# Performance work log

Measured on AMD Instinct MI355X. Metric: run time of the kernel, lower is better.

Reference implementation:

```python
import jax, jax.numpy as jnp
import numpy as np

T, B = 64, 512
X, H, Z, A = 1024, 1024, 256, 64


def setup_inputs() -> dict:
    key = jax.random.key(0)
    ks = jax.random.split(key, 24)
    s = 0.02
    n = lambda k, shape: (jax.random.normal(k, shape, dtype=jnp.float32) * s)
    d = {
        "obs_seq": jax.random.normal(ks[0], (T, B, X), dtype=jnp.float32),
        "act_seq": jax.random.normal(ks[1], (T, B, A), dtype=jnp.float32),
        "eps": jax.random.normal(ks[2], (T, B, Z), dtype=jnp.float32),
        # Transition: aggr Linear(z+a -> h), GRUCell(h, h)
        "aggr_W": n(ks[3], (Z + A, H)), "aggr_b": jnp.zeros((H,), jnp.float32),
        "gru_Wih": n(ks[4], (H, 3 * H)), "gru_Whh": n(ks[5], (H, 3 * H)),
        "gru_bih": jnp.zeros((3 * H,), jnp.float32), "gru_bhh": jnp.zeros((3 * H,), jnp.float32),
        # z_q_dist: NormalPredictor(x+h -> hidden h -> z)
        "q_W1": n(ks[6], (X + H, H)), "q_b1": jnp.zeros((H,), jnp.float32),
        "q_Wm": n(ks[7], (H, Z)), "q_bm": jnp.zeros((Z,), jnp.float32),
        "q_Ws": n(ks[8], (H, Z)), "q_bs": jnp.zeros((Z,), jnp.float32),
        # z_p_dist: NormalPredictor(h -> hidden h -> z)
        "p_W1": n(ks[9], (H, H)), "p_b1": jnp.zeros((H,), jnp.float32),
        "p_Wm": n(ks[10], (H, Z)), "p_bm": jnp.zeros((Z,), jnp.float32),
        "p_Ws": n(ks[11], (H, Z)), "p_bs": jnp.zeros((Z,), jnp.float32),
    }
    return d


def _gru_cell(x, h, Wih, Whh, bih, bhh):
    # torch.nn.GRUCell math
    gi = x @ Wih + bih
    gh = h @ Whh + bhh
    i_r, i_z, i_n = jnp.split(gi, 3, axis=-1)
    h_r, h_z, h_n = jnp.split(gh, 3, axis=-1)
    r = jax.nn.sigmoid(i_r + h_r)
    z = jax.nn.sigmoid(i_z + h_z)
    n = jnp.tanh(i_n + r * h_n)
    return (1.0 - z) * n + z * h


def _normal_predictor(x, W1, b1, Wm, bm, Ws, bs):
    hid = jax.nn.elu(x @ W1 + b1)
    loc = hid @ Wm + bm
    scale = jax.nn.softplus(hid @ Ws + bs)
    return loc, scale


def reference(obs_seq, act_seq, eps, aggr_W, aggr_b, gru_Wih, gru_Whh, gru_bih,
              gru_bhh, q_W1, q_b1, q_Wm, q_bm, q_Ws, q_bs, p_W1, p_b1, p_Wm,
              p_bm, p_Ws, p_bs):
    batch = obs_seq.shape[1]
    h0 = jnp.zeros((batch, gru_Whh.shape[0]), dtype=obs_seq.dtype)

    def step(h, inp):
        obs, act, e = inp
        q_loc, q_scale = _normal_predictor(
            jnp.concatenate([obs, h], axis=-1), q_W1, q_b1, q_Wm, q_bm, q_Ws, q_bs)
        z_q = q_loc + q_scale * e  # rsample
        p_loc, p_scale = _normal_predictor(h, p_W1, p_b1, p_Wm, p_bm, p_Ws, p_bs)
        a = jax.nn.elu(jnp.concatenate([z_q, act], axis=-1) @ aggr_W + aggr_b)
        h_new = _gru_cell(a, h, gru_Wih, gru_Whh, gru_bih, gru_bhh)
        return h_new, (h_new, q_loc, q_scale, p_loc, p_scale, z_q)

    _, (bel, q_loc, q_scale, p_loc, p_scale, z_qs) = jax.lax.scan(
        step, h0, (obs_seq, act_seq, eps))
    beliefs = jnp.concatenate([h0[None], bel], axis=0)  # [T+1, B, H]
    return beliefs, (q_loc, q_scale), (p_loc, p_scale), z_qs
```

## Files before the change

### kernel.cpp

```cpp
#include <hip/hip_runtime.h>
#include <hip/hip_bf16.h>
#include <stdint.h>

#define TT 64
#define BB 512
#define XX 1024
#define HH 1024
#define ZZ 256
#define AA 64

typedef __bf16 bf16;
typedef bf16 bf16x8 __attribute__((ext_vector_type(8)));
typedef float f32x4 __attribute__((ext_vector_type(4)));

#define SZ_BEL ((long)(TT + 1) * BB * HH)
#define SZ_TBZ ((long)TT * BB * ZZ)
#define OFF_QL (SZ_BEL)
#define OFF_QS (OFF_QL + SZ_TBZ)
#define OFF_PL (OFF_QL + 2 * SZ_TBZ)
#define OFF_PS (OFF_QL + 3 * SZ_TBZ)
#define OFF_ZQ (OFF_QL + 4 * SZ_TBZ)

#define GLL16(g, l)                                                         \
  __builtin_amdgcn_global_load_lds(                                         \
      (__attribute__((address_space(1))) void*)(g),                         \
      (__attribute__((address_space(3))) void*)(l), 16, 0, 0)

__device__ __forceinline__ float eluf(float x) {
  return x > 0.f ? x : expf(x) - 1.f;
}
__device__ __forceinline__ float splusf(float x) {
  return fmaxf(x, 0.f) + log1pf(expf(-fabsf(x)));
}
__device__ __forceinline__ float sigf(float x) {
  return 1.f / (1.f + expf(-x));
}

struct GArgs {
  const bf16* A; const float* Af; const bf16* A2;
  long lda, lda2; int ksplit;
  const bf16* Bt;
  int M, N, K, t;
  const float *b_q1, *b_ghh, *b_ag, *b_p1, *b_pm, *b_ps;
  const bf16* obs_pre;
  bf16 *hid_q, *a_buf, *out_bf;
  float *gh, *dout;
};

template <int BM, int BN, int EPI, bool AF32>
__global__ __launch_bounds__(256) void gemm_k(GArgs g) {
  constexpr int BK = 32;
  constexpr int WTM = BM / 2, WTN = BN / 2;
  constexpr int MR = WTM / 16, NR = WTN / 16;
  constexpr int CA = BM * 4 / 256, CB = BN * 4 / 256;
  __shared__ bf16 sA[BM * BK];
  __shared__ bf16 sB[BN * BK];
  const int nbm = g.M / BM;
  const int bm = blockIdx.x % nbm, bn = blockIdx.x / nbm;
  const int m0 = bm * BM, n0 = bn * BN;
  const int tid = threadIdx.x;
  const int wid = tid >> 6, lane = tid & 63;
  const int wm = wid & 1, wn = wid >> 1;
  const int lr = lane & 15, lk = lane >> 4;

  f32x4 acc[MR][NR] = {};

  for (int k0 = 0; k0 < g.K; k0 += BK) {
    __syncthreads();
    if constexpr (AF32) {
#pragma unroll
      for (int i = 0; i < CA; i++) {
        int c = tid + i * 256, row = c >> 2, kc = c & 3;
        const float* s = g.Af + (long)(m0 + row) * g.lda + k0 + kc * 8;
        float4 v0 = *(const float4*)s;
        float4 v1 = *(const float4*)(s + 4);
        bf16x8 p;
        p[0] = (bf16)v0.x; p[1] = (bf16)v0.y; p[2] = (bf16)v0.z; p[3] = (bf16)v0.w;
        p[4] = (bf16)v1.x; p[5] = (bf16)v1.y; p[6] = (bf16)v1.z; p[7] = (bf16)v1.w;
        *(bf16x8*)&sA[c * 8] = p;
      }
    } else {
#pragma unroll
      for (int i = 0; i < CA; i++) {
        int c = tid + i * 256, row = c >> 2, kc = c & 3;
        const bf16* s;
        if (EPI == 3 && k0 >= g.ksplit)
          s = g.A2 + (long)(m0 + row) * g.lda2 + (k0 - g.ksplit) + kc * 8;
        else
          s = g.A + (long)(m0 + row) * g.lda + k0 + kc * 8;
        GLL16(s, &sA[c * 8]);
      }
    }
#pragma unroll
    for (int i = 0; i < CB; i++) {
      int c = tid + i * 256, row = c >> 2, kc = c & 3;
      GLL16(g.Bt + (long)(n0 + row) * g.K + k0 + kc * 8, &sB[c * 8]);
    }
    __syncthreads();
    bf16x8 af[MR];
#pragma unroll
    for (int mi = 0; mi < MR; mi++)
      af[mi] = *(const bf16x8*)&sA[(wm * WTM + mi * 16 + lr) * BK + lk * 8];
#pragma unroll
    for (int nj = 0; nj < NR; nj++) {
      bf16x8 bfr = *(const bf16x8*)&sB[(wn * WTN + nj * 16 + lr) * BK + lk * 8];
#pragma unroll
      for (int mi = 0; mi < MR; mi++)
        acc[mi][nj] = __builtin_amdgcn_mfma_f32_16x16x32_bf16(af[mi], bfr, acc[mi][nj], 0, 0, 0);
    }
  }

#pragma unroll
  for (int mi = 0; mi < MR; mi++) {
#pragma unroll
    for (int nj = 0; nj < NR; nj++) {
#pragma unroll
      for (int r = 0; r < 4; r++) {
        const int row = m0 + wm * WTM + mi * 16 + lk * 4 + r;
        const int col = n0 + wn * WTN + nj * 16 + lr;
        float v = acc[mi][nj][r];
        if constexpr (EPI == 0) {
          g.out_bf[(long)row * g.N + col] = (bf16)v;
        } else if constexpr (EPI == 1) {
          if (col < HH) {
            float x = v + g.b_q1[col] + (float)g.obs_pre[((long)g.t * BB + row) * HH + col];
            g.hid_q[row * HH + col] = (bf16)eluf(x);
          } else {
            int j = col - HH;
            g.gh[(long)row * 3 * HH + j] = v + g.b_ghh[j];
          }
        } else if constexpr (EPI == 3) {
          g.a_buf[row * HH + col] = (bf16)eluf(v + g.b_ag[col]);
        } else if constexpr (EPI == 5) {
          g.out_bf[(long)row * g.N + col] = (bf16)eluf(v + g.b_p1[col]);
        } else {
          int region = col >> 8, j = col & 255;
          float x = v + (region ? g.b_ps[j] : g.b_pm[j]);
          if (region) x = splusf(x);
          g.dout[(region ? OFF_PS : OFF_PL) + (long)row * ZZ + j] = x;
        }
      }
    }
  }
}

struct QZArgs {
  const bf16* A; const bf16* Bt2;
  const float *b_qm, *b_qs; const float* eps;
  float* dout; bf16* z_bf; int t;
};
__global__ __launch_bounds__(256) void qz_gemm(QZArgs g) {
  constexpr int BK = 32;
  __shared__ bf16 sA[64 * BK];
  __shared__ bf16 sB[256 * BK];
  const int bm = blockIdx.x & 7, bn = blockIdx.x >> 3;
  const int m0 = bm * 64, n0 = bn * 128;
  const int tid = threadIdx.x;
  const int wid = tid >> 6, lane = tid & 63;
  const int wm = wid & 1, wn = wid >> 1;
  const int lr = lane & 15, lk = lane >> 4;

  f32x4 accL[2][4] = {}, accS[2][4] = {};

  for (int k0 = 0; k0 < HH; k0 += BK) {
    __syncthreads();
    {
      int c = tid, row = c >> 2, kc = c & 3;
      GLL16(g.A + (long)(m0 + row) * HH + k0 + kc * 8, &sA[c * 8]);
    }
#pragma unroll
    for (int i = 0; i < 4; i++) {
      int c = tid + i * 256, row = c >> 2, kc = c & 3;
      int grow = (row < 128) ? (n0 + row) : (256 + n0 + (row - 128));
      GLL16(g.Bt2 + (long)grow * HH + k0 + kc * 8, &sB[c * 8]);
    }
    __syncthreads();
    bf16x8 af[2];
#pragma unroll
    for (int mi = 0; mi < 2; mi++)
      af[mi] = *(const bf16x8*)&sA[(wm * 32 + mi * 16 + lr) * BK + lk * 8];
#pragma unroll
    for (int nj = 0; nj < 4; nj++) {
      bf16x8 bL = *(const bf16x8*)&sB[(wn * 64 + nj * 16 + lr) * BK + lk * 8];
      bf16x8 bS = *(const bf16x8*)&sB[(128 + wn * 64 + nj * 16 + lr) * BK + lk * 8];
#pragma unroll
      for (int mi = 0; mi < 2; mi++) {
        accL[mi][nj] = __builtin_amdgcn_mfma_f32_16x16x32_bf16(af[mi], bL, accL[mi][nj], 0, 0, 0);
        accS[mi][nj] = __builtin_amdgcn_mfma_f32_16x16x32_bf16(af[mi], bS, accS[mi][nj], 0, 0, 0);
      }
    }
  }

#pragma unroll
  for (int mi = 0; mi < 2; mi++) {
#pragma unroll
    for (int nj = 0; nj < 4; nj++) {
#pragma unroll
      for (int r = 0; r < 4; r++) {
        const int row = m0 + wm * 32 + mi * 16 + lk * 4 + r;
        const int j = n0 + wn * 64 + nj * 16 + lr;
        long o = ((long)g.t * BB + row) * ZZ + j;
        float loc = accL[mi][nj][r] + g.b_qm[j];
        float sc = splusf(accS[mi][nj][r] + g.b_qs[j]);
        float z = loc + sc * g.eps[o];
        g.dout[OFF_QL + o] = loc;
        g.dout[OFF_QS + o] = sc;
        g.dout[OFF_ZQ + o] = z;
        g.z_bf[row * ZZ + j] = (bf16)z;
      }
    }
  }
}

struct GRUArgs {
  const bf16* A; const bf16* Bt;
  const float* b_gih; const float* gh;
  bf16* h_bf; float* dout; int t;
};
__global__ __launch_bounds__(256) void gru_gemm(GRUArgs g) {
  constexpr int BK = 32;
  __shared__ bf16 sA[64 * BK];
  __shared__ bf16 sB[192 * BK];
  const int bm = blockIdx.x & 7, bn = blockIdx.x >> 3;
  const int m0 = bm * 64, n0 = bn * 64;
  const int tid = threadIdx.x;
  const int wid = tid >> 6, lane = tid & 63;
  const int wm = wid & 1, wn = wid >> 1;
  const int lr = lane & 15, lk = lane >> 4;

  f32x4 acc[2][3][2] = {};

  for (int k0 = 0; k0 < HH; k0 += BK) {
    __syncthreads();
    {
      int c = tid, row = c >> 2, kc = c & 3;
      GLL16(g.A + (long)(m0 + row) * HH + k0 + kc * 8, &sA[c * 8]);
    }
#pragma unroll
    for (int i = 0; i < 3; i++) {
      int c = tid + i * 256, row = c >> 2, kc = c & 3;
      int gate = row >> 6, jr = row & 63;
      GLL16(g.Bt + (long)(gate * HH + n0 + jr) * HH + k0 + kc * 8, &sB[c * 8]);
    }
    __syncthreads();
    bf16x8 af[2];
#pragma unroll
    for (int mi = 0; mi < 2; mi++)
      af[mi] = *(const bf16x8*)&sA[(wm * 32 + mi * 16 + lr) * BK + lk * 8];
#pragma unroll
    for (int gt = 0; gt < 3; gt++) {
#pragma unroll
      for (int nj = 0; nj < 2; nj++) {
        bf16x8 bfr = *(const bf16x8*)&sB[(gt * 64 + wn * 32 + nj * 16 + lr) * BK + lk * 8];
#pragma unroll
        for (int mi = 0; mi < 2; mi++)
          acc[mi][gt][nj] = __builtin_amdgcn_mfma_f32_16x16x32_bf16(af[mi], bfr, acc[mi][gt][nj], 0, 0, 0);
      }
    }
  }

#pragma unroll
  for (int mi = 0; mi < 2; mi++) {
#pragma unroll
    for (int nj = 0; nj < 2; nj++) {
#pragma unroll
      for (int r = 0; r < 4; r++) {
        const int row = m0 + wm * 32 + mi * 16 + lk * 4 + r;
        const int j = n0 + wn * 32 + nj * 16 + lr;
        const long gb = (long)row * 3 * HH + j;
        float gir = acc[mi][0][nj][r] + g.b_gih[j];
        float giz = acc[mi][1][nj][r] + g.b_gih[HH + j];
        float gin = acc[mi][2][nj][r] + g.b_gih[2 * HH + j];
        float rr = sigf(gir + g.gh[gb]);
        float zz = sigf(giz + g.gh[gb + HH]);
        float nn = tanhf(gin + rr * g.gh[gb + 2 * HH]);
        float h = (float)g.h_bf[row * HH + j];
        float hn = (1.f - zz) * nn + zz * h;
        g.h_bf[row * HH + j] = (bf16)hn;
        g.dout[(long)(g.t + 1) * BB * HH + (long)row * HH + j] = hn;
      }
    }
  }
}

__global__ void transpose_cvt(const float* __restrict__ src, bf16* __restrict__ dst,
                              int K, int N, int ld, int k_off) {
  __shared__ float tile[32][33];
  const int nb = blockIdx.x * 32, kb = blockIdx.y * 32;
  const int tx = threadIdx.x, ty = threadIdx.y;
#pragma unroll
  for (int j = 0; j < 32; j += 8)
    tile[ty + j][tx] = src[(long)(kb + ty + j + k_off) * ld + nb + tx];
  __syncthreads();
#pragma unroll
  for (int j = 0; j < 32; j += 8)
    dst[(long)(nb + ty + j) * K + kb + tx] = (bf16)tile[tx][ty + j];
}

__global__ void cvt_bf16(const float* __restrict__ src, bf16* __restrict__ dst, long n) {
  long i = ((long)blockIdx.x * blockDim.x + threadIdx.x) * 4;
  if (i < n) {
    float4 v = *(const float4*)(src + i);
    dst[i] = (bf16)v.x; dst[i + 1] = (bf16)v.y;
    dst[i + 2] = (bf16)v.z; dst[i + 3] = (bf16)v.w;
  }
}

__global__ void init_k(bf16* hbf, float* dout) {
  int i = blockIdx.x * 256 + threadIdx.x;
  hbf[i] = (bf16)0.f;
  dout[i] = 0.f;
}

extern "C" void kernel_launch(void* const* d_in, const int* in_sizes, int n_in,
                              void* d_out, int out_size, void* d_ws, size_t ws_size,
                              hipStream_t stream) {
  const float* obs  = (const float*)d_in[0];
  const float* act  = (const float*)d_in[1];
  const float* eps  = (const float*)d_in[2];
  const float* aggrW = (const float*)d_in[3];
  const float* aggrB = (const float*)d_in[4];
  const float* gWih = (const float*)d_in[5];
  const float* gWhh = (const float*)d_in[6];
  const float* gbih = (const float*)d_in[7];
  const float* gbhh = (const float*)d_in[8];
  const float* qW1  = (const float*)d_in[9];
  const float* qb1  = (const float*)d_in[10];
  const float* qWm  = (const float*)d_in[11];
  const float* qbm  = (const float*)d_in[12];
  const float* qWs  = (const float*)d_in[13];
  const float* qbs  = (const float*)d_in[14];
  const float* pW1  = (const float*)d_in[15];
  const float* pb1  = (const float*)d_in[16];
  const float* pWm  = (const float*)d_in[17];
  const float* pbm  = (const float*)d_in[18];
  const float* pWs  = (const float*)d_in[19];
  const float* pbs  = (const float*)d_in[20];
  float* dout = (float*)d_out;

  char* w = (char*)d_ws;
  size_t off = 0;
  auto alloc = [&](size_t bytes) -> char* {
    char* r = w + off;
    off = (off + bytes + 255) & ~(size_t)255;
    return r;
  };
  bf16* WT_qobs = (bf16*)alloc((size_t)XX * HH * 2);
  bf16* WT_h   = (bf16*)alloc((size_t)4096 * 1024 * 2);
  bf16* WT_qh  = (bf16*)alloc((size_t)512 * 1024 * 2);
  bf16* WT_ag  = (bf16*)alloc((size_t)1024 * 320 * 2);
  bf16* WT_ih  = (bf16*)alloc((size_t)3072 * 1024 * 2);
  bf16* WT_p1  = (bf16*)alloc((size_t)1024 * 1024 * 2);
  bf16* WT_ph  = (bf16*)alloc((size_t)512 * 1024 * 2);
  bf16* obs_pre = (bf16*)alloc((size_t)TT * BB * HH * 2);
  bf16* p_hid  = obs_pre;
  bf16* act_bf = (bf16*)alloc((size_t)TT * BB * AA * 2);
  bf16* h_bf   = (bf16*)alloc((size_t)BB * HH * 2);
  bf16* hid_q  = (bf16*)alloc((size_t)BB * HH * 2);
  bf16* z_bf   = (bf16*)alloc((size_t)BB * ZZ * 2);
  bf16* a_buf  = (bf16*)alloc((size_t)BB * HH * 2);
  float* gh_f  = (float*)alloc((size_t)BB * 3 * HH * 4);
  (void)ws_size; (void)in_sizes; (void)n_in; (void)out_size;

  dim3 tb(32, 8);
  transpose_cvt<<<dim3(32, 32), tb, 0, stream>>>(qW1, WT_qobs, 1024, 1024, 1024, 0);
  transpose_cvt<<<dim3(32, 32), tb, 0, stream>>>(qW1, WT_h, 1024, 1024, 1024, 1024);
  transpose_cvt<<<dim3(96, 32), tb, 0, stream>>>(gWhh, WT_h + 1024 * 1024, 1024, 3072, 3072, 0);
  transpose_cvt<<<dim3(8, 32), tb, 0, stream>>>(qWm, WT_qh, 1024, 256, 256, 0);
  transpose_cvt<<<dim3(8, 32), tb, 0, stream>>>(qWs, WT_qh + 256 * 1024, 1024, 256, 256, 0);
  transpose_cvt<<<dim3(32, 10), tb, 0, stream>>>(aggrW, WT_ag, 320, 1024, 1024, 0);
  transpose_cvt<<<dim3(96, 32), tb, 0, stream>>>(gWih, WT_ih, 1024, 3072, 3072, 0);
  transpose_cvt<<<dim3(32, 32), tb, 0, stream>>>(pW1, WT_p1, 1024, 1024, 1024, 0);
  transpose_cvt<<<dim3(8, 32), tb, 0, stream>>>(pWm, WT_ph, 1024, 256, 256, 0);
  transpose_cvt<<<dim3(8, 32), tb, 0, stream>>>(pWs, WT_ph + 256 * 1024, 1024, 256, 256, 0);
  cvt_bf16<<<TT * BB * AA / 4 / 256, 256, 0, stream>>>(act, act_bf, (long)TT * BB * AA);
  init_k<<<BB * HH / 256, 256, 0, stream>>>(h_bf, dout);

  GArgs g{};
  g.b_q1 = qb1; g.b_ghh = gbhh; g.b_ag = aggrB; g.b_p1 = pb1;
  g.b_pm = pbm; g.b_ps = pbs;
  g.obs_pre = obs_pre; g.hid_q = hid_q; g.a_buf = a_buf;
  g.gh = gh_f; g.dout = dout;

  {
    GArgs a = g;
    a.Af = obs; a.lda = XX; a.Bt = WT_qobs;
    a.M = TT * BB; a.N = HH; a.K = XX; a.out_bf = obs_pre;
    gemm_k<128, 128, 0, true><<<(TT * BB / 128) * (HH / 128), 256, 0, stream>>>(a);
  }

  for (int t = 0; t < TT; ++t) {
    {
      GArgs a = g; a.t = t;
      a.A = h_bf; a.lda = HH; a.Bt = WT_h;
      a.M = BB; a.N = 4096; a.K = HH;
      gemm_k<64, 128, 1, false><<<(BB / 64) * (4096 / 128), 256, 0, stream>>>(a);
    }
    {
      QZArgs a{hid_q, WT_qh, qbm, qbs, eps, dout, z_bf, t};
      qz_gemm<<<8 * 2, 256, 0, stream>>>(a);
    }
    {
      GArgs a = g; a.t = t;
      a.A = z_bf; a.lda = ZZ;
      a.A2 = act_bf + (size_t)t * BB * AA; a.lda2 = AA; a.ksplit = ZZ;
      a.Bt = WT_ag; a.M = BB; a.N = 1024; a.K = ZZ + AA;
      gemm_k<64, 128, 3, false><<<(BB / 64) * (1024 / 128), 256, 0, stream>>>(a);
    }
    {
      GRUArgs a{a_buf, WT_ih, gbih, gh_f, h_bf, dout, t};
      gru_gemm<<<8 * 16, 256, 0, stream>>>(a);
    }
  }

  {
    GArgs a = g;
    a.Af = dout; a.lda = HH; a.Bt = WT_p1;
    a.M = TT * BB; a.N = HH; a.K = HH; a.out_bf = p_hid;
    gemm_k<128, 128, 5, true><<<(TT * BB / 128) * (HH / 128), 256, 0, stream>>>(a);
  }
  {
    GArgs a = g;
    a.A = p_hid; a.lda = HH; a.Bt = WT_ph;
    a.M = TT * BB; a.N = 512; a.K = HH;
    gemm_k<128, 128, 6, false><<<(TT * BB / 128) * (512 / 128), 256, 0, stream>>>(a);
  }
}
```

Baseline: 7.323 ms.

## Fuse recurrent scan into one persistent kernel with grid barriers

Replaces the 256 per-timestep kernel launches of the recurrent loop with a single persistent kernel of 256 blocks that uses an atomic grid-wide barrier between the four GEMM stages of each step. The GEMMs also switch to BK=64 double-buffered LDS staging with an XOR swizzle, and the tiling is redistributed across the 256 blocks. This targets launch overhead and the idle gaps between small dependent kernels. In exchange it relies on all 256 blocks being co-resident, since the spin barrier deadlocks otherwise, and the qz and aggr stages leave most blocks idle.

```diff
diff --git a/kernel.cpp b/kernel.cpp
--- a/kernel.cpp
+++ b/kernel.cpp
@@ -8,6 +8,9 @@
 #define HH 1024
 #define ZZ 256
 #define AA 64
+
+#define NBLK 256
+#define NTHR 512
 
 typedef __bf16 bf16;
 typedef bf16 bf16x8 __attribute__((ext_vector_type(8)));
@@ -26,25 +29,288 @@
       (__attribute__((address_space(1))) void*)(g),                         \
       (__attribute__((address_space(3))) void*)(l), 16, 0, 0)
 
-__device__ __forceinline__ float eluf(float x) {
-  return x > 0.f ? x : expf(x) - 1.f;
-}
-__device__ __forceinline__ float splusf(float x) {
-  return fmaxf(x, 0.f) + log1pf(expf(-fabsf(x)));
-}
-__device__ __forceinline__ float sigf(float x) {
-  return 1.f / (1.f + expf(-x));
-}
+#define MFMA(a, b, c) __builtin_amdgcn_mfma_f32_16x16x32_bf16(a, b, c, 0, 0, 0)
+
+__device__ __forceinline__ float eluf(float x) { return x > 0.f ? x : expf(x) - 1.f; }
+__device__ __forceinline__ float splusf(float x) { return fmaxf(x, 0.f) + log1pf(expf(-fabsf(x))); }
+__device__ __forceinline__ float sigf(float x) { return 1.f / (1.f + expf(-x)); }
+
+
+struct ScanArgs {
+  const bf16 *WT_h, *WT_qh, *WT_ag, *WT_ih;
+  const bf16 *obs_pre, *act_bf;
+  bf16 *h_bf, *hid_q, *z_bf, *a_buf;
+  float* gh;
+  const float *b_q1, *b_ghh, *b_qm, *b_qs, *b_ag, *b_gih;
+  const float* eps;
+  float* dout;
+  unsigned* bar;
+};
+
+__device__ __forceinline__ void gsync(unsigned* bar, unsigned& gen) {
+  __syncthreads();
+  if (threadIdx.x == 0) {
+    __threadfence();
+    atomicAdd(bar, 1u);
+    unsigned tgt = (++gen) * NBLK;
+    while (__hip_atomic_load(bar, __ATOMIC_RELAXED, __HIP_MEMORY_SCOPE_AGENT) < tgt)
+      __builtin_amdgcn_s_sleep(8);
+  }
+  __syncthreads();
+  __threadfence();
+}
+
+__device__ __forceinline__ bf16x8 ldfrag(const bf16* buf, int row, int w) {
+  return *(const bf16x8*)((const char*)buf + row * 128 + (w ^ ((row & 7) << 4)));
+}
+
+__device__ __forceinline__ void stage_rows(const bf16* base, long ld, int k0,
+                                           char* lds, int nrows) {
+  for (int c = threadIdx.x; c < nrows * 8; c += NTHR) {
+    int row = c >> 3, cb = (c & 7) << 4;
+    int scb = (cb ^ ((row & 7) << 4)) >> 1;
+    GLL16(base + (long)row * ld + k0 + scb, lds + c * 16);
+  }
+}
+
+__global__ __launch_bounds__(NTHR, 4) void scan_k(ScanArgs s) {
+  __shared__ char smem[49152];
+  bf16* sA = (bf16*)smem;
+  bf16* sB = (bf16*)(smem + 16384);
+  const int bid = blockIdx.x, tid = threadIdx.x;
+  const int wid = tid >> 6, lane = tid & 63;
+  const int lr = lane & 15, lk = lane >> 4;
+  unsigned gen = 0;
+
+  for (int t = 0; t < TT; ++t) {
+    {
+      const int m = bid >> 5, n = bid & 31;
+      const int m0 = m * 64, n0 = n * 128;
+      const int wm = wid & 1, wn = wid >> 1;
+      const bf16* Ag = s.h_bf + (long)m0 * HH;
+      const bf16* Bg = s.WT_h + (long)n0 * HH;
+      f32x4 acc[2][2] = {};
+      stage_rows(Ag, HH, 0, (char*)sA, 64);
+      stage_rows(Bg, HH, 0, (char*)sB, 128);
+      __syncthreads();
+      for (int kt = 0; kt < 16; ++kt) {
+        int cur = kt & 1;
+        if (kt < 15) {
+          stage_rows(Ag, HH, (kt + 1) * 64, (char*)(sA + (cur ^ 1) * 4096), 64);
+          stage_rows(Bg, HH, (kt + 1) * 64, (char*)(sB + (cur ^ 1) * 8192), 128);
+        }
+        const bf16* Ab = sA + cur * 4096;
+        const bf16* Bb = sB + cur * 8192;
+#pragma unroll
+        for (int ks = 0; ks < 2; ++ks) {
+          int w = ks * 64 + lk * 16;
+          bf16x8 a0 = ldfrag(Ab, wm * 32 + lr, w);
+          bf16x8 a1 = ldfrag(Ab, wm * 32 + 16 + lr, w);
+          bf16x8 b0 = ldfrag(Bb, wn * 32 + lr, w);
+          bf16x8 b1 = ldfrag(Bb, wn * 32 + 16 + lr, w);
+          acc[0][0] = MFMA(a0, b0, acc[0][0]);
+          acc[0][1] = MFMA(a0, b1, acc[0][1]);
+          acc[1][0] = MFMA(a1, b0, acc[1][0]);
+          acc[1][1] = MFMA(a1, b1, acc[1][1]);
+        }
+        __syncthreads();
+      }
+#pragma unroll
+      for (int mi = 0; mi < 2; mi++)
+#pragma unroll
+        for (int nj = 0; nj < 2; nj++)
+#pragma unroll
+          for (int r = 0; r < 4; r++) {
+            int row = m0 + wm * 32 + mi * 16 + lk * 4 + r;
+            int col = n0 + wn * 32 + nj * 16 + lr;
+            float v = acc[mi][nj][r];
+            if (n0 < HH) {
+              float x = v + s.b_q1[col] + (float)s.obs_pre[((long)t * BB + row) * HH + col];
+              s.hid_q[row * HH + col] = (bf16)eluf(x);
+            } else {
+              int j = col - HH;
+              s.gh[(long)row * 3 * HH + j] = v + s.b_ghh[j];
+            }
+          }
+    }
+    gsync(s.bar, gen);
+
+    if (bid < 32) {
+      const int m = bid >> 2, n = bid & 3;
+      const int m0 = m * 64, n0 = n * 64;
+      const int wm = wid & 1, wn = wid >> 1;
+      const bf16* Ag = s.hid_q + (long)m0 * HH;
+      f32x4 accL[2] = {}, accS[2] = {};
+      stage_rows(Ag, HH, 0, (char*)sA, 64);
+      for (int c = tid; c < 1024; c += NTHR) {
+        int row = c >> 3, cb = (c & 7) << 4;
+        int scb = (cb ^ ((row & 7) << 4)) >> 1;
+        int brow = (row < 64) ? (n0 + row) : (192 + n0 + row);
+        GLL16(s.WT_qh + (long)brow * HH + scb, (char*)sB + c * 16);
+      }
+      __syncthreads();
+      for (int kt = 0; kt < 16; ++kt) {
+        int cur = kt & 1;
+        if (kt < 15) {
+          stage_rows(Ag, HH, (kt + 1) * 64, (char*)(sA + (cur ^ 1) * 4096), 64);
+          for (int c = tid; c < 1024; c += NTHR) {
+            int row = c >> 3, cb = (c & 7) << 4;
+            int scb = (cb ^ ((row & 7) << 4)) >> 1;
+            int brow = (row < 64) ? (n0 + row) : (192 + n0 + row);
+            GLL16(s.WT_qh + (long)brow * HH + (kt + 1) * 64 + scb,
+                  (char*)(sB + (cur ^ 1) * 8192) + c * 16);
+          }
+        }
+        const bf16* Ab = sA + cur * 4096;
+        const bf16* Bb = sB + cur * 8192;
+#pragma unroll
+        for (int ks = 0; ks < 2; ++ks) {
+          int w = ks * 64 + lk * 16;
+          bf16x8 a0 = ldfrag(Ab, wm * 32 + lr, w);
+          bf16x8 a1 = ldfrag(Ab, wm * 32 + 16 + lr, w);
+          bf16x8 bl = ldfrag(Bb, wn * 16 + lr, w);
+          bf16x8 bs = ldfrag(Bb, 64 + wn * 16 + lr, w);
+          accL[0] = MFMA(a0, bl, accL[0]);
+          accL[1] = MFMA(a1, bl, accL[1]);
+          accS[0] = MFMA(a0, bs, accS[0]);
+          accS[1] = MFMA(a1, bs, accS[1]);
+        }
+        __syncthreads();
+      }
+#pragma unroll
+      for (int mi = 0; mi < 2; mi++)
+#pragma unroll
+        for (int r = 0; r < 4; r++) {
+          int row = m0 + wm * 32 + mi * 16 + lk * 4 + r;
+          int j = n0 + wn * 16 + lr;
+          long o = ((long)t * BB + row) * ZZ + j;
+          float loc = accL[mi][r] + s.b_qm[j];
+          float sc = splusf(accS[mi][r] + s.b_qs[j]);
+          float z = loc + sc * s.eps[o];
+          s.dout[OFF_QL + o] = loc;
+          s.dout[OFF_QS + o] = sc;
+          s.dout[OFF_ZQ + o] = z;
+          s.z_bf[row * ZZ + j] = (bf16)z;
+        }
+    }
+    gsync(s.bar, gen);
+
+    if (bid < 128) {
+      const int m = bid >> 4, n = bid & 15;
+      const int m0 = m * 64, n0 = n * 64;
+      const int wm = wid & 1, wn = wid >> 1;
+      const bf16* Bg = s.WT_ag + (long)n0 * 320;
+      f32x4 acc[2] = {};
+      auto stageA3 = [&](int ktn, char* dst) {
+        int c = tid;
+        int row = c >> 3, cb = (c & 7) << 4;
+        int scb = (cb ^ ((row & 7) << 4)) >> 1;
+        const bf16* src = (ktn < 4)
+            ? s.z_bf + (long)(m0 + row) * ZZ + ktn * 64 + scb
+            : s.act_bf + (long)t * BB * AA + (long)(m0 + row) * AA + scb;
+        GLL16(src, dst + c * 16);
+      };
+      stageA3(0, (char*)sA);
+      stage_rows(Bg, 320, 0, (char*)sB, 64);
+      __syncthreads();
+      for (int kt = 0; kt < 5; ++kt) {
+        int cur = kt & 1;
+        if (kt < 4) {
+          stageA3(kt + 1, (char*)(sA + (cur ^ 1) * 4096));
+          stage_rows(Bg, 320, (kt + 1) * 64, (char*)(sB + (cur ^ 1) * 8192), 64);
+        }
+        const bf16* Ab = sA + cur * 4096;
+        const bf16* Bb = sB + cur * 8192;
+#pragma unroll
+        for (int ks = 0; ks < 2; ++ks) {
+          int w = ks * 64 + lk * 16;
+          bf16x8 a0 = ldfrag(Ab, wm * 32 + lr, w);
+          bf16x8 a1 = ldfrag(Ab, wm * 32 + 16 + lr, w);
+          bf16x8 b = ldfrag(Bb, wn * 16 + lr, w);
+          acc[0] = MFMA(a0, b, acc[0]);
+          acc[1] = MFMA(a1, b, acc[1]);
+        }
+        __syncthreads();
+      }
+#pragma unroll
+      for (int mi = 0; mi < 2; mi++)
+#pragma unroll
+        for (int r = 0; r < 4; r++) {
+          int row = m0 + wm * 32 + mi * 16 + lk * 4 + r;
+          int col = n0 + wn * 16 + lr;
+          s.a_buf[row * HH + col] = (bf16)eluf(acc[mi][r] + s.b_ag[col]);
+        }
+    }
+    gsync(s.bar, gen);
+
+    {
+      const int m = bid >> 5, jb = bid & 31;
+      const int m0 = m * 64, j0 = jb * 32;
+      const int wm4 = wid & 3, wn2 = wid >> 2;
+      const bf16* Ag = s.a_buf + (long)m0 * HH;
+      f32x4 acc[3] = {};
+      auto stageB4 = [&](int k0, char* dst) {
+        for (int c = tid; c < 768; c += NTHR) {
+          int row = c >> 3, cb = (c & 7) << 4;
+          int scb = (cb ^ ((row & 7) << 4)) >> 1;
+          int brow = (row >> 5) * HH + j0 + (row & 31);
+          GLL16(s.WT_ih + (long)brow * HH + k0 + scb, dst + c * 16);
+        }
+      };
+      stage_rows(Ag, HH, 0, (char*)sA, 64);
+      stageB4(0, (char*)sB);
+      __syncthreads();
+      for (int kt = 0; kt < 16; ++kt) {
+        int cur = kt & 1;
+        if (kt < 15) {
+          stage_rows(Ag, HH, (kt + 1) * 64, (char*)(sA + (cur ^ 1) * 4096), 64);
+          stageB4((kt + 1) * 64, (char*)(sB + (cur ^ 1) * 8192));
+        }
+        const bf16* Ab = sA + cur * 4096;
+        const bf16* Bb = sB + cur * 8192;
+#pragma unroll
+        for (int ks = 0; ks < 2; ++ks) {
+          int w = ks * 64 + lk * 16;
+          bf16x8 a = ldfrag(Ab, wm4 * 16 + lr, w);
+          bf16x8 b0 = ldfrag(Bb, wn2 * 16 + lr, w);
+          bf16x8 b1 = ldfrag(Bb, 32 + wn2 * 16 + lr, w);
+          bf16x8 b2 = ldfrag(Bb, 64 + wn2 * 16 + lr, w);
+          acc[0] = MFMA(a, b0, acc[0]);
+          acc[1] = MFMA(a, b1, acc[1]);
+          acc[2] = MFMA(a, b2, acc[2]);
+        }
+        __syncthreads();
+      }
+#pragma unroll
+      for (int r = 0; r < 4; r++) {
+        int row = m0 + wm4 * 16 + lk * 4 + r;
+        int j = j0 + wn2 * 16 + lr;
+        long gb = (long)row * 3 * HH + j;
+        float gir = acc[0][r] + s.b_gih[j] + s.gh[gb];
+        float giz = acc[1][r] + s.b_gih[HH + j] + s.gh[gb + HH];
+        float gin = acc[2][r] + s.b_gih[2 * HH + j];
+        float rr = sigf(gir);
+        float zz = sigf(giz);
+        float nn = tanhf(gin + rr * s.gh[gb + 2 * HH]);
+        float h = (float)s.h_bf[row * HH + j];
+        float hn = (1.f - zz) * nn + zz * h;
+        s.h_bf[row * HH + j] = (bf16)hn;
+        s.dout[(long)(t + 1) * BB * HH + (long)row * HH + j] = hn;
+      }
+    }
+    gsync(s.bar, gen);
+  }
+}
+
 
 struct GArgs {
-  const bf16* A; const float* Af; const bf16* A2;
-  long lda, lda2; int ksplit;
+  const bf16* A; const float* Af;
+  long lda;
   const bf16* Bt;
-  int M, N, K, t;
-  const float *b_q1, *b_ghh, *b_ag, *b_p1, *b_pm, *b_ps;
-  const bf16* obs_pre;
-  bf16 *hid_q, *a_buf, *out_bf;
-  float *gh, *dout;
+  int M, N, K;
+  const float *b_p1, *b_pm, *b_ps;
+  bf16* out_bf;
+  float* dout;
 };
 
 template <int BM, int BN, int EPI, bool AF32>
@@ -71,9 +337,9 @@
 #pragma unroll
       for (int i = 0; i < CA; i++) {
         int c = tid + i * 256, row = c >> 2, kc = c & 3;
-        const float* s = g.Af + (long)(m0 + row) * g.lda + k0 + kc * 8;
-        float4 v0 = *(const float4*)s;
-        float4 v1 = *(const float4*)(s + 4);
+        const float* sp = g.Af + (long)(m0 + row) * g.lda + k0 + kc * 8;
+        float4 v0 = *(const float4*)sp;
+        float4 v1 = *(const float4*)(sp + 4);
         bf16x8 p;
         p[0] = (bf16)v0.x; p[1] = (bf16)v0.y; p[2] = (bf16)v0.z; p[3] = (bf16)v0.w;
         p[4] = (bf16)v1.x; p[5] = (bf16)v1.y; p[6] = (bf16)v1.z; p[7] = (bf16)v1.w;
@@ -83,12 +349,7 @@
 #pragma unroll
       for (int i = 0; i < CA; i++) {
         int c = tid + i * 256, row = c >> 2, kc = c & 3;
-        const bf16* s;
-        if (EPI == 3 && k0 >= g.ksplit)
-          s = g.A2 + (long)(m0 + row) * g.lda2 + (k0 - g.ksplit) + kc * 8;
-        else
-          s = g.A + (long)(m0 + row) * g.lda + k0 + kc * 8;
-        GLL16(s, &sA[c * 8]);
+        GLL16(g.A + (long)(m0 + row) * g.lda + k0 + kc * 8, &sA[c * 8]);
       }
     }
 #pragma unroll
@@ -106,14 +367,14 @@
       bf16x8 bfr = *(const bf16x8*)&sB[(wn * WTN + nj * 16 + lr) * BK + lk * 8];
 #pragma unroll
       for (int mi = 0; mi < MR; mi++)
-        acc[mi][nj] = __builtin_amdgcn_mfma_f32_16x16x32_bf16(af[mi], bfr, acc[mi][nj], 0, 0, 0);
-    }
-  }
-
-#pragma unroll
-  for (int mi = 0; mi < MR; mi++) {
-#pragma unroll
-    for (int nj = 0; nj < NR; nj++) {
+        acc[mi][nj] = MFMA(af[mi], bfr, acc[mi][nj]);
+    }
+  }
+
+#pragma unroll
+  for (int mi = 0; mi < MR; mi++)
+#pragma unroll
+    for (int nj = 0; nj < NR; nj++)
 #pragma unroll
       for (int r = 0; r < 4; r++) {
         const int row = m0 + wm * WTM + mi * 16 + lk * 4 + r;
@@ -121,16 +382,6 @@
         float v = acc[mi][nj][r];
         if constexpr (EPI == 0) {
           g.out_bf[(long)row * g.N + col] = (bf16)v;
-        } else if constexpr (EPI == 1) {
-          if (col < HH) {
-            float x = v + g.b_q1[col] + (float)g.obs_pre[((long)g.t * BB + row) * HH + col];
-            g.hid_q[row * HH + col] = (bf16)eluf(x);
-          } else {
-            int j = col - HH;
-            g.gh[(long)row * 3 * HH + j] = v + g.b_ghh[j];
-          }
-        } else if constexpr (EPI == 3) {
-          g.a_buf[row * HH + col] = (bf16)eluf(v + g.b_ag[col]);
         } else if constexpr (EPI == 5) {
           g.out_bf[(long)row * g.N + col] = (bf16)eluf(v + g.b_p1[col]);
         } else {
@@ -140,147 +391,6 @@
           g.dout[(region ? OFF_PS : OFF_PL) + (long)row * ZZ + j] = x;
         }
       }
-    }
-  }
-}
-
-struct QZArgs {
-  const bf16* A; const bf16* Bt2;
-  const float *b_qm, *b_qs; const float* eps;
-  float* dout; bf16* z_bf; int t;
-};
-__global__ __launch_bounds__(256) void qz_gemm(QZArgs g) {
-  constexpr int BK = 32;
-  __shared__ bf16 sA[64 * BK];
-  __shared__ bf16 sB[256 * BK];
-  const int bm = blockIdx.x & 7, bn = blockIdx.x >> 3;
-  const int m0 = bm * 64, n0 = bn * 128;
-  const int tid = threadIdx.x;
-  const int wid = tid >> 6, lane = tid & 63;
-  const int wm = wid & 1, wn = wid >> 1;
-  const int lr = lane & 15, lk = lane >> 4;
-
-  f32x4 accL[2][4] = {}, accS[2][4] = {};
-
-  for (int k0 = 0; k0 < HH; k0 += BK) {
-    __syncthreads();
-    {
-      int c = tid, row = c >> 2, kc = c & 3;
-      GLL16(g.A + (long)(m0 + row) * HH + k0 + kc * 8, &sA[c * 8]);
-    }
-#pragma unroll
-    for (int i = 0; i < 4; i++) {
-      int c = tid + i * 256, row = c >> 2, kc = c & 3;
-      int grow = (row < 128) ? (n0 + row) : (256 + n0 + (row - 128));
-      GLL16(g.Bt2 + (long)grow * HH + k0 + kc * 8, &sB[c * 8]);
-    }
-    __syncthreads();
-    bf16x8 af[2];
-#pragma unroll
-    for (int mi = 0; mi < 2; mi++)
-      af[mi] = *(const bf16x8*)&sA[(wm * 32 + mi * 16 + lr) * BK + lk * 8];
-#pragma unroll
-    for (int nj = 0; nj < 4; nj++) {
-      bf16x8 bL = *(const bf16x8*)&sB[(wn * 64 + nj * 16 + lr) * BK + lk * 8];
-      bf16x8 bS = *(const bf16x8*)&sB[(128 + wn * 64 + nj * 16 + lr) * BK + lk * 8];
-#pragma unroll
-      for (int mi = 0; mi < 2; mi++) {
-        accL[mi][nj] = __builtin_amdgcn_mfma_f32_16x16x32_bf16(af[mi], bL, accL[mi][nj], 0, 0, 0);
-        accS[mi][nj] = __builtin_amdgcn_mfma_f32_16x16x32_bf16(af[mi], bS, accS[mi][nj], 0, 0, 0);
-      }
-    }
-  }
-
-#pragma unroll
-  for (int mi = 0; mi < 2; mi++) {
-#pragma unroll
-    for (int nj = 0; nj < 4; nj++) {
-#pragma unroll
-      for (int r = 0; r < 4; r++) {
-        const int row = m0 + wm * 32 + mi * 16 + lk * 4 + r;
-        const int j = n0 + wn * 64 + nj * 16 + lr;
-        long o = ((long)g.t * BB + row) * ZZ + j;
-        float loc = accL[mi][nj][r] + g.b_qm[j];
-        float sc = splusf(accS[mi][nj][r] + g.b_qs[j]);
-        float z = loc + sc * g.eps[o];
-        g.dout[OFF_QL + o] = loc;
-        g.dout[OFF_QS + o] = sc;
-        g.dout[OFF_ZQ + o] = z;
-        g.z_bf[row * ZZ + j] = (bf16)z;
-      }
-    }
-  }
-}
-
-struct GRUArgs {
-  const bf16* A; const bf16* Bt;
-  const float* b_gih; const float* gh;
-  bf16* h_bf; float* dout; int t;
-};
-__global__ __launch_bounds__(256) void gru_gemm(GRUArgs g) {
-  constexpr int BK = 32;
-  __shared__ bf16 sA[64 * BK];
-  __shared__ bf16 sB[192 * BK];
-  const int bm = blockIdx.x & 7, bn = blockIdx.x >> 3;
-  const int m0 = bm * 64, n0 = bn * 64;
-  const int tid = threadIdx.x;
-  const int wid = tid >> 6, lane = tid & 63;
-  const int wm = wid & 1, wn = wid >> 1;
-  const int lr = lane & 15, lk = lane >> 4;
-
-  f32x4 acc[2][3][2] = {};
-
-  for (int k0 = 0; k0 < HH; k0 += BK) {
-    __syncthreads();
-    {
-      int c = tid, row = c >> 2, kc = c & 3;
-      GLL16(g.A + (long)(m0 + row) * HH + k0 + kc * 8, &sA[c * 8]);
-    }
-#pragma unroll
-    for (int i = 0; i < 3; i++) {
-      int c = tid + i * 256, row = c >> 2, kc = c & 3;
-      int gate = row >> 6, jr = row & 63;
-      GLL16(g.Bt + (long)(gate * HH + n0 + jr) * HH + k0 + kc * 8, &sB[c * 8]);
-    }
-    __syncthreads();
-    bf16x8 af[2];
-#pragma unroll
-    for (int mi = 0; mi < 2; mi++)
-      af[mi] = *(const bf16x8*)&sA[(wm * 32 + mi * 16 + lr) * BK + lk * 8];
-#pragma unroll
-    for (int gt = 0; gt < 3; gt++) {
-#pragma unroll
-      for (int nj = 0; nj < 2; nj++) {
-        bf16x8 bfr = *(const bf16x8*)&sB[(gt * 64 + wn * 32 + nj * 16 + lr) * BK + lk * 8];
-#pragma unroll
-        for (int mi = 0; mi < 2; mi++)
-          acc[mi][gt][nj] = __builtin_amdgcn_mfma_f32_16x16x32_bf16(af[mi], bfr, acc[mi][gt][nj], 0, 0, 0);
-      }
-    }
-  }
-
-#pragma unroll
-  for (int mi = 0; mi < 2; mi++) {
-#pragma unroll
-    for (int nj = 0; nj < 2; nj++) {
-#pragma unroll
-      for (int r = 0; r < 4; r++) {
-        const int row = m0 + wm * 32 + mi * 16 + lk * 4 + r;
-        const int j = n0 + wn * 32 + nj * 16 + lr;
-        const long gb = (long)row * 3 * HH + j;
-        float gir = acc[mi][0][nj][r] + g.b_gih[j];
-        float giz = acc[mi][1][nj][r] + g.b_gih[HH + j];
-        float gin = acc[mi][2][nj][r] + g.b_gih[2 * HH + j];
-        float rr = sigf(gir + g.gh[gb]);
-        float zz = sigf(giz + g.gh[gb + HH]);
-        float nn = tanhf(gin + rr * g.gh[gb + 2 * HH]);
-        float h = (float)g.h_bf[row * HH + j];
-        float hn = (1.f - zz) * nn + zz * h;
-        g.h_bf[row * HH + j] = (bf16)hn;
-        g.dout[(long)(g.t + 1) * BB * HH + (long)row * HH + j] = hn;
-      }
-    }
-  }
 }
 
 __global__ void transpose_cvt(const float* __restrict__ src, bf16* __restrict__ dst,
@@ -360,7 +470,10 @@
   bf16* z_bf   = (bf16*)alloc((size_t)BB * ZZ * 2);
   bf16* a_buf  = (bf16*)alloc((size_t)BB * HH * 2);
   float* gh_f  = (float*)alloc((size_t)BB * 3 * HH * 4);
+  unsigned* bar = (unsigned*)alloc(256);
   (void)ws_size; (void)in_sizes; (void)n_in; (void)out_size;
+
+  hipMemsetAsync(bar, 0, 256, stream);
 
   dim3 tb(32, 8);
   transpose_cvt<<<dim3(32, 32), tb, 0, stream>>>(qW1, WT_qobs, 1024, 1024, 1024, 0);
@@ -376,53 +489,36 @@
   cvt_bf16<<<TT * BB * AA / 4 / 256, 256, 0, stream>>>(act, act_bf, (long)TT * BB * AA);
   init_k<<<BB * HH / 256, 256, 0, stream>>>(h_bf, dout);
 
-  GArgs g{};
-  g.b_q1 = qb1; g.b_ghh = gbhh; g.b_ag = aggrB; g.b_p1 = pb1;
-  g.b_pm = pbm; g.b_ps = pbs;
-  g.obs_pre = obs_pre; g.hid_q = hid_q; g.a_buf = a_buf;
-  g.gh = gh_f; g.dout = dout;
-
   {
-    GArgs a = g;
+    GArgs a{};
     a.Af = obs; a.lda = XX; a.Bt = WT_qobs;
     a.M = TT * BB; a.N = HH; a.K = XX; a.out_bf = obs_pre;
     gemm_k<128, 128, 0, true><<<(TT * BB / 128) * (HH / 128), 256, 0, stream>>>(a);
   }
 
-  for (int t = 0; t < TT; ++t) {
-    {
-      GArgs a = g; a.t = t;
-      a.A = h_bf; a.lda = HH; a.Bt = WT_h;
-      a.M = BB; a.N = 4096; a.K = HH;
-      gemm_k<64, 128, 1, false><<<(BB / 64) * (4096 / 128), 256, 0, stream>>>(a);
-    }
-    {
-      QZArgs a{hid_q, WT_qh, qbm, qbs, eps, dout, z_bf, t};
-      qz_gemm<<<8 * 2, 256, 0, stream>>>(a);
-    }
-    {
-      GArgs a = g; a.t = t;
-      a.A = z_bf; a.lda = ZZ;
-      a.A2 = act_bf + (size_t)t * BB * AA; a.lda2 = AA; a.ksplit = ZZ;
-      a.Bt = WT_ag; a.M = BB; a.N = 1024; a.K = ZZ + AA;
-      gemm_k<64, 128, 3, false><<<(BB / 64) * (1024 / 128), 256, 0, stream>>>(a);
-    }
-    {
-      GRUArgs a{a_buf, WT_ih, gbih, gh_f, h_bf, dout, t};
-      gru_gemm<<<8 * 16, 256, 0, stream>>>(a);
-    }
-  }
-
   {
-    GArgs a = g;
+    ScanArgs s{};
+    s.WT_h = WT_h; s.WT_qh = WT_qh; s.WT_ag = WT_ag; s.WT_ih = WT_ih;
+    s.obs_pre = obs_pre; s.act_bf = act_bf;
+    s.h_bf = h_bf; s.hid_q = hid_q; s.z_bf = z_bf; s.a_buf = a_buf;
+    s.gh = gh_f;
+    s.b_q1 = qb1; s.b_ghh = gbhh; s.b_qm = qbm; s.b_qs = qbs;
+    s.b_ag = aggrB; s.b_gih = gbih;
+    s.eps = eps; s.dout = dout; s.bar = bar;
+    scan_k<<<NBLK, NTHR, 0, stream>>>(s);
+  }
+
+  {
+    GArgs a{};
     a.Af = dout; a.lda = HH; a.Bt = WT_p1;
-    a.M = TT * BB; a.N = HH; a.K = HH; a.out_bf = p_hid;
+    a.M = TT * BB; a.N = HH; a.K = HH; a.out_bf = p_hid; a.b_p1 = pb1;
     gemm_k<128, 128, 5, true><<<(TT * BB / 128) * (HH / 128), 256, 0, stream>>>(a);
   }
   {
-    GArgs a = g;
+    GArgs a{};
     a.A = p_hid; a.lda = HH; a.Bt = WT_ph;
     a.M = TT * BB; a.N = 512; a.K = HH;
+    a.b_pm = pbm; a.b_ps = pbs; a.dout = dout;
     gemm_k<128, 128, 6, false><<<(TT * BB / 128) * (512 / 128), 256, 0, stream>>>(a);
   }
 }
```

New measurement: 17.33 ms. 137% more time.
